# Kernel tuning notes

Hardware: AMD Instinct MI355X
Metric: run time of the kernel (lower is better)

Reference implementation:

```python
import jax, jax.numpy as jnp
import numpy as np

CR = 64                      # cond_repeat
DILS = tuple(2 ** i for _ in range(2) for i in range(10))  # 2 blocks x 10 layers
Q_ZERO = 128


def setup_inputs() -> dict:
    key = jax.random.key(0)
    B, C, TE = 8, 64, 8          # batch, cond channels, encoding timesteps
    R, S, Q = 128, 128, 256      # residual, skip, classes
    L = len(DILS)
    ks = jax.random.split(key, 12)
    sc = 0.1
    return {
        "encodings": jax.random.normal(ks[0], (B, C, TE), jnp.float32),
        "first_w": jax.random.normal(ks[1], (R, 1, 2), jnp.float32) * sc,
        "first_b": jnp.zeros((R,), jnp.float32),
        "causal_w": jax.random.normal(ks[2], (L, 2 * R, R, 2), jnp.float32) * sc,
        "causal_b": jnp.zeros((L, 2 * R), jnp.float32),
        "cond_w": jax.random.normal(ks[3], (L, 2 * R, C), jnp.float32) * sc,
        "cond_b": jnp.zeros((L, 2 * R), jnp.float32),
        "res_w": jax.random.normal(ks[4], (L, R, R), jnp.float32) * sc,
        "res_b": jnp.zeros((L, R), jnp.float32),
        "skip_w": jax.random.normal(ks[5], (L, S, R), jnp.float32) * sc,
        "skip_b": jnp.zeros((L, S), jnp.float32),
        "skipc_w": jax.random.normal(ks[6], (S, R), jnp.float32) * sc,
        "skipc_b": jnp.zeros((S,), jnp.float32),
        "fc_w": jax.random.normal(ks[7], (S, S), jnp.float32) * sc,
        "fc_b": jnp.zeros((S,), jnp.float32),
        "condf_w": jax.random.normal(ks[8], (S, C), jnp.float32) * sc,
        "condf_b": jnp.zeros((S,), jnp.float32),
        "logits_w": jax.random.normal(ks[9], (Q, S), jnp.float32) * sc,
        "logits_b": jnp.zeros((Q,), jnp.float32),
    }


def _generate(encodings, first_w, first_b, causal_w, causal_b, cond_w, cond_b,
              res_w, res_b, skip_w, skip_b, skipc_w, skipc_b, fc_w, fc_b,
              condf_w, condf_b, logits_w, logits_b):
    B = encodings.shape[0]
    R = res_w.shape[1]
    T = encodings.shape[2] * CR

    # ring buffers emulate QueuedConv1d (queue length = dilation, zero-initialized)
    buf_first0 = jnp.zeros((B, 1), jnp.float32)
    bufs0 = tuple(jnp.zeros((B, d, R), jnp.float32) for d in DILS)
    sample0 = jnp.full((B,), Q_ZERO, jnp.int32)

    def step(carry, t):
        sample, buf_first, bufs = carry
        x = sample.astype(jnp.float32) / 255.0 - 0.5                      # [B]
        c = jax.lax.dynamic_index_in_dim(encodings, t // CR, axis=2,
                                         keepdims=False)                  # [B,C]
        # first causal conv (1 -> R, kernel 2): tap0 on delayed sample, tap1 on current
        prev0 = buf_first[:, 0]
        buf_first = buf_first.at[:, 0].set(x)
        res = (prev0[:, None] * first_w[None, :, 0, 0]
               + x[:, None] * first_w[None, :, 0, 1] + first_b)           # [B,R]
        skip = res @ skipc_w.T + skipc_b                                  # [B,S]
        new_bufs = []
        for l, d in enumerate(DILS):
            idx = jnp.mod(t, d)
            prev = jax.lax.dynamic_index_in_dim(bufs[l], idx, axis=1, keepdims=False)
            new_bufs.append(jax.lax.dynamic_update_index_in_dim(bufs[l], res, idx, axis=1))
            z = (prev @ causal_w[l, :, :, 0].T + res @ causal_w[l, :, :, 1].T
                 + causal_b[l] + c @ cond_w[l].T + cond_b[l])             # [B,2R]
            gate, out = jnp.split(z, 2, axis=1)
            h = jax.nn.sigmoid(gate) * jnp.tanh(out)                      # [B,R]
            res = res + h @ res_w[l].T + res_b[l]
            skip = skip + h @ skip_w[l].T + skip_b[l]
        s = jax.nn.relu(skip) @ fc_w.T + fc_b + c @ condf_w.T + condf_b
        logits = jax.nn.relu(s) @ logits_w.T + logits_b                   # [B,Q]
        sample = jnp.argmax(logits, axis=1).astype(jnp.int32)             # 'max' sampling
        return (sample, buf_first, tuple(new_bufs)), (sample, logits)

    _, (samples, logits) = jax.lax.scan(step, (sample0, buf_first0, bufs0),
                                        jnp.arange(T))
    return samples, logits  # [T,B] int32, [T,B,Q] float32


def reference(encodings, first_w, first_b, causal_w, causal_b, cond_w, cond_b,
              res_w, res_b, skip_w, skip_b, skipc_w, skipc_b, fc_w, fc_b,
              condf_w, condf_b, logits_w, logits_b):
    return _generate(encodings, first_w, first_b, causal_w, causal_b, cond_w, cond_b,
                     res_w, res_b, skip_w, skip_b, skipc_w, skipc_b, fc_w, fc_b,
                     condf_w, condf_b, logits_w, logits_b)
```

## Files before the change

### kernel.cpp

```cpp
#include <hip/hip_runtime.h>
#include <math.h>

#define BB 8
#define TT 512
#define LL 20
#define NBLK 64
#define NTHR 256

typedef float f4 __attribute__((ext_vector_type(4)));
typedef unsigned long long ull;

__constant__ int c_dil[LL] = {1,2,4,8,16,32,64,128,256,512,
                              1,2,4,8,16,32,64,128,256,512};
__constant__ int c_roff[LL] = {-1,0,4096,12288,28672,61440,126976,258048,520192,1044480,
                               2093056,2095104,2099200,2107392,2123776,2156544,
                               2222080,2353152,2615296,3139584};

constexpr size_t OFF_RING = 0;
constexpr size_t OFF_X    = 4188160;

#define P_WC     0
#define P_F      20480
#define P_WST    30208
#define P_WSKIPC 30720
#define P_WFC    30976
#define P_WLOG   31232
#define P_WF0    31744
#define P_WF1    31872
#define P_FB     32000
#define P_CONDZ  32128
#define P_SFC    32768
#define P_RESB   32784
#define P_SKIPB  32824
#define P_ZB     32864
#define P_LOGB   32944
#define P_SKIPCB 32948
#define P_XCUR   32950
#define P_XPREV  32958
#define P_XNEW   32966
#define P_SZ     32976
#define P_SL     33008
#define P_SKACC  33040
#define P_R2     33056
#define P_CF     33072
#define P_PREVF  33600
#define P_HF     34656
#define P_RESF   35712
#define P_RES0   36768
#define POOL_FL  38880

__device__ __forceinline__ f4 ldx(const f4* p) {
    f4 r;
    asm volatile("global_load_dwordx4 %0, %1, off sc0 sc1\n\ts_waitcnt vmcnt(0)"
                 : "=v"(r) : "v"(p) : "memory");
    return r;
}
__device__ __forceinline__ void ldx2(const f4* p0, const f4* p1, f4& a, f4& b) {
    asm volatile("global_load_dwordx4 %0, %2, off sc0 sc1\n\t"
                 "global_load_dwordx4 %1, %3, off sc0 sc1\n\t"
                 "s_waitcnt vmcnt(0)"
                 : "=v"(a), "=v"(b) : "v"(p0), "v"(p1) : "memory");
}
__device__ __forceinline__ void stx(f4* p, f4 v) {
    asm volatile("s_waitcnt vmcnt(0)\n\t"
                 "global_store_dwordx4 %0, %1, off sc0 sc1"
                 :: "v"(p), "v"(v) : "memory");
}

__device__ __forceinline__ void publish16(f4* slot, int J, const float* sl, int e) {
    if (threadIdx.x < 6) {
        int q = threadIdx.x;
        f4 v;
        v.x = sl[3*q];
        v.y = (3*q+1 < 16) ? sl[3*q+1] : 0.f;
        v.z = (3*q+2 < 16) ? sl[3*q+2] : 0.f;
        v.w = __int_as_float(e);
        stx(slot + J*6 + q, v);
    }
}
__device__ __forceinline__ void scat16(float* dst, f4 v, int vi, bool dorelu) {
    int j = vi / 6, q = vi - 6*j;
    #pragma unroll
    for (int i = 0; i < 3; ++i) {
        int E = 3*q + i;
        if (E < 16) {
            float x = v[i];
            if (dorelu) x = fmaxf(x, 0.f);
            dst[(E & 7)*132 + 2*j + (E >> 3)] = x;
        }
    }
}
__device__ __forceinline__ void consume16(const f4* slot, int e, float* dst, bool dorelu) {
    int m = threadIdx.x;
    const f4 *p0 = slot + m, *p1 = slot + 256 + m;
    f4 a, b;
    bool two = (m < 128);
    if (two) ldx2(p0, p1, a, b); else a = ldx(p0);
    while (__float_as_int(a.w) != e) { __builtin_amdgcn_s_sleep(1); a = ldx(p0); }
    if (two) { while (__float_as_int(b.w) != e) { __builtin_amdgcn_s_sleep(1); b = ldx(p1); } }
    scat16(dst, a, m, dorelu);
    if (two) scat16(dst, b, m + 256, dorelu);
}
__device__ __forceinline__ void publish32(f4* slot, int J, const float* sl, int e) {
    if (threadIdx.x < 11) {
        int q = threadIdx.x;
        f4 v;
        v.x = sl[3*q];
        v.y = (3*q+1 < 32) ? sl[3*q+1] : 0.f;
        v.z = (3*q+2 < 32) ? sl[3*q+2] : 0.f;
        v.w = __int_as_float(e);
        stx(slot + J*11 + q, v);
    }
}
__device__ __forceinline__ void scat32(float* dst, f4 v, int vi) {
    int j = vi / 11, q = vi - 11*j;
    #pragma unroll
    for (int i = 0; i < 3; ++i) {
        int E = 3*q + i;
        if (E < 32) dst[(E & 7)*260 + 4*j + (E >> 3)] = v[i];
    }
}
__device__ __forceinline__ void consume32(const f4* slot, int e, float* dst) {
    int m = threadIdx.x;
    const f4 *p0 = slot + m, *p1 = slot + 256 + m, *p2 = slot + 512 + m;
    f4 a, b, c;
    ldx2(p0, p1, a, b);
    bool three = (m < 192);
    if (three) c = ldx(p2);
    while (__float_as_int(a.w) != e) { __builtin_amdgcn_s_sleep(1); a = ldx(p0); }
    while (__float_as_int(b.w) != e) { __builtin_amdgcn_s_sleep(1); b = ldx(p1); }
    if (three) { while (__float_as_int(c.w) != e) { __builtin_amdgcn_s_sleep(1); c = ldx(p2); } }
    scat32(dst, a, m);
    scat32(dst, b, m + 256);
    if (three) scat32(dst, c, m + 512);
}

__global__ __launch_bounds__(NTHR, 1) void wn_gen(
    const float* __restrict__ enc,
    const float* __restrict__ first_w,  const float* __restrict__ first_b,
    const float* __restrict__ causal_w, const float* __restrict__ causal_b,
    const float* __restrict__ cond_w,   const float* __restrict__ cond_b,
    const float* __restrict__ res_w,    const float* __restrict__ res_b,
    const float* __restrict__ skip_w,   const float* __restrict__ skip_b,
    const float* __restrict__ skipc_w,  const float* __restrict__ skipc_b,
    const float* __restrict__ fc_w,     const float* __restrict__ fc_b,
    const float* __restrict__ condf_w,  const float* __restrict__ condf_b,
    const float* __restrict__ logits_w, const float* __restrict__ logits_b,
    float* __restrict__ wsf, float* __restrict__ out)
{
    extern __shared__ float pool[];
    const int tid = threadIdx.x;
    const int J = blockIdx.x;
    float* ring = wsf + OFF_RING;
    f4* xb = (f4*)(wsf + OFF_X);

    for (int m = tid; m < 20480; m += NTHR) {
        int l = m >> 10, rem = m & 1023, g = rem >> 8, i = rem & 255;
        int grow = (g < 2) ? (2*J + g) : (128 + 2*J + (g - 2));
        int col = i & 127, k = i >> 7;
        pool[P_WC + m] = causal_w[((size_t)(l*256 + grow)*128 + col)*2 + k];
    }
    if (tid < 256) {
        int r = tid >> 7, i = tid & 127;
        pool[P_WSKIPC + tid] = skipc_w[(size_t)(2*J + r)*128 + i];
        pool[P_WFC + tid]    = fc_w[(size_t)(2*J + r)*128 + i];
    }
    for (int m = tid; m < 512; m += NTHR) {
        int w = m >> 7, i = m & 127;
        pool[P_WLOG + m] = logits_w[(size_t)(4*J + w)*128 + i];
    }
    if (tid < 128) {
        pool[P_WF0 + tid] = first_w[2*tid];
        pool[P_WF1 + tid] = first_w[2*tid + 1];
        pool[P_FB + tid]  = first_b[tid];
    }
    if (tid < 40) {
        int l = tid >> 1, r = tid & 1;
        pool[P_RESB + tid]  = res_b[l*128 + 2*J + r];
        pool[P_SKIPB + tid] = skip_b[l*128 + 2*J + r];
    }
    if (tid < 4) pool[P_LOGB + tid] = logits_b[4*J + tid];
    if (tid < 2) pool[P_SKIPCB + tid] = skipc_b[2*J + tid];
    for (int m = tid; m < 2112; m += NTHR) pool[P_RES0 + m] = 0.f;
    if (tid < 8) { pool[P_XCUR + tid] = 128.f/255.f - 0.5f; pool[P_XPREV + tid] = 0.f; }
    __syncthreads();

    for (int l = 0; l < 19; ++l) {
        for (int m = tid; m < 512; m += NTHR) {
            int g = m >> 7, j = m & 127;
            const float* w1 = pool + P_WC + ((l+1)*4 + g)*256 + 128;
            const float* rw = res_w + (size_t)l*128*128 + j;
            float acc = 0.f;
            #pragma unroll 8
            for (int i = 0; i < 128; ++i) acc += w1[i] * rw[(size_t)i*128];
            pool[P_F + (l*4 + g)*128 + j] = acc;
        }
    }
    if (tid < 80) {
        int l = tid >> 2, g = tid & 3;
        float acc = 0.f;
        if (l >= 1) {
            const float* w1 = pool + P_WC + (l*4 + g)*256 + 128;
            for (int i = 0; i < 128; ++i) acc += w1[i] * res_b[(l-1)*128 + i];
        }
        pool[P_ZB + tid] = acc;
    }
    __syncthreads();

    int e = 0;
    int er_pending = 0;

    for (int t = 0; t < TT; ++t) {
        if ((t & 63) == 0) {
            int te = t >> 6;
            for (int m = tid; m < 512; m += NTHR) {
                int b = m >> 6, j = m & 63;
                pool[P_CF + b*66 + j] = enc[(size_t)b*512 + j*8 + te];
            }
            __syncthreads();
            for (int m = tid; m < 640; m += NTHR) {
                int l = m >> 5, rem = m & 31, g = rem >> 3, b = rem & 7;
                int grow = (g < 2) ? (2*J + g) : (128 + 2*J + (g - 2));
                float acc = causal_b[l*256 + grow] + cond_b[l*256 + grow]
                          + pool[P_ZB + l*4 + g];
                const float* cw = cond_w + (size_t)(l*256 + grow)*64;
                const float* cf = pool + P_CF + b*66;
                for (int j = 0; j < 64; ++j) acc += cw[j]*cf[j];
                pool[P_CONDZ + l*32 + g*8 + b] = acc;
            }
            if (tid < 16) {
                int r = tid >> 3, b = tid & 7, row = 2*J + r;
                float acc = fc_b[row] + condf_b[row];
                const float* cw = condf_w + (size_t)row*64;
                const float* cf = pool + P_CF + b*66;
                for (int j = 0; j < 64; ++j) acc += cw[j]*cf[j];
                pool[P_SFC + r*8 + b] = acc;
            }
            __syncthreads();
        }

        const int cur = t & 1;
        for (int m = tid; m < 1024; m += NTHR) {
            int b = m >> 7, r = m & 127;
            pool[P_RES0 + cur*1056 + b*132 + r] =
                pool[P_XPREV + b]*pool[P_WF0 + r] + pool[P_XCUR + b]*pool[P_WF1 + r] + pool[P_FB + r];
        }
        __syncthreads();
        {
            int w = tid >> 6, lane = tid & 63, b = lane >> 3, k = lane & 7;
            if (w < 2) {
                const float* wr = pool + P_WSKIPC + w*128;
                const float* rs = pool + P_RES0 + cur*1056 + b*132;
                float acc = 0.f;
                #pragma unroll
                for (int i = 0; i < 16; ++i) { int j = k + 8*i; acc += wr[j]*rs[j]; }
                acc += __shfl_xor(acc,1); acc += __shfl_xor(acc,2); acc += __shfl_xor(acc,4);
                if (k == 0) pool[P_SKACC + w*8 + b] = acc + pool[P_SKIPCB + w];
            }
        }
        if (tid < 16) {
            int r = tid >> 3, b = tid & 7;
            pool[P_R2 + r*8 + b] = pool[P_RES0 + cur*1056 + b*132 + 2*J + r];
        }

        for (int l = 0; l < LL; ++l) {
            {
                int g = tid >> 6, lane = tid & 63, b = lane >> 3, k = lane & 7;
                const float* w0 = pool + P_WC + (l*4 + g)*256;
                const float* pv = ((l == 0) ? pool + P_RES0 + (cur^1)*1056 : pool + P_PREVF) + b*132;
                const float* rs = ((l <= 1) ? pool + P_RES0 + cur*1056 : pool + P_RESF) + b*132;
                float acc = 0.f;
                #pragma unroll
                for (int i = 0; i < 16; ++i) {
                    int j = k + 8*i;
                    acc += w0[j]*pv[j] + w0[128 + j]*rs[j];
                }
                if (l >= 1) {
                    const float* fm = pool + P_F + ((l-1)*4 + g)*128;
                    const float* hh = pool + P_HF + b*132;
                    #pragma unroll
                    for (int i = 0; i < 16; ++i) { int j = k + 8*i; acc += fm[j]*hh[j]; }
                }
                acc += __shfl_xor(acc,1); acc += __shfl_xor(acc,2); acc += __shfl_xor(acc,4);
                if (k == 0) pool[P_SZ + g*8 + b] = acc;
            }
            __syncthreads();
            if (tid < 16) {
                int r = tid & 1, b = tid >> 1;
                float g = pool[P_SZ + r*8 + b]     + pool[P_CONDZ + l*32 + r*8 + b];
                float o = pool[P_SZ + (2+r)*8 + b] + pool[P_CONDZ + l*32 + (2+r)*8 + b];
                pool[P_SL + r*8 + b] = (1.f/(1.f + expf(-g))) * tanhf(o);
            }
            __syncthreads();
            ++e; int eh = e;
            publish16(xb + (size_t)(eh & 3)*768, J, pool + P_SL, eh);
            float wv0, wv1;
            {
                int r0 = tid >> 7, i0 = tid & 127;
                wv0 = res_w [(size_t)(l*128 + 2*J + r0)*128 + i0];
                wv1 = skip_w[(size_t)(l*128 + 2*J + r0)*128 + i0];
            }
            ull pfa = 0, pfb = 0;
            if (l <= 18) {
                int d = c_dil[l+1];
                if (t >= d) {
                    int slot = (t - d) & (2*d - 1);
                    const float* rp = ring + c_roff[l+1] + (size_t)slot*1024 + tid*4;
                    pfa = __hip_atomic_load((const ull*)rp,     __ATOMIC_RELAXED, __HIP_MEMORY_SCOPE_AGENT);
                    pfb = __hip_atomic_load((const ull*)(rp+2), __ATOMIC_RELAXED, __HIP_MEMORY_SCOPE_AGENT);
                }
            }
            if (l >= 1 && l <= 18)
                consume16(xb + (size_t)(er_pending & 3)*768, er_pending, pool + P_RESF, false);
            consume16(xb + (size_t)(eh & 3)*768, eh, pool + P_HF, false);
            pool[P_WST + tid] = wv0;
            pool[P_WST + 256 + tid] = wv1;
            __syncthreads();
            {
                int w = tid >> 6, lane = tid & 63, b = lane >> 3, k = lane & 7;
                int r = w & 1, isSkip = w >> 1;
                if (isSkip || l <= 18) {
                    const float* wr = pool + P_WST + (isSkip ? 256 : 0) + r*128;
                    const float* hh = pool + P_HF + b*132;
                    float acc = 0.f;
                    #pragma unroll
                    for (int i = 0; i < 16; ++i) { int j = k + 8*i; acc += wr[j]*hh[j]; }
                    acc += __shfl_xor(acc,1); acc += __shfl_xor(acc,2); acc += __shfl_xor(acc,4);
                    if (k == 0) {
                        if (isSkip) {
                            pool[P_SKACC + r*8 + b] += acc + pool[P_SKIPB + l*2 + r];
                        } else {
                            float v = pool[P_R2 + r*8 + b] + acc + pool[P_RESB + l*2 + r];
                            pool[P_R2 + r*8 + b] = v;
                            pool[P_SL + r*8 + b] = v;
                            int d = c_dil[l+1];
                            int slot = t & (2*d - 1);
                            float* wp = ring + c_roff[l+1] + (size_t)slot*1024 + b*128 + 2*J + r;
                            __hip_atomic_store(wp, v, __ATOMIC_RELAXED, __HIP_MEMORY_SCOPE_AGENT);
                        }
                    }
                }
            }
            __syncthreads();
            if (l <= 17) {
                ++e;
                publish16(xb + (size_t)(e & 3)*768, J, pool + P_SL, e);
                er_pending = e;
            }
            if (l <= 18) {
                int b = tid >> 5, c = (tid & 31)*4;
                union { ull u; float f[2]; } u0, u1;
                u0.u = pfa; u1.u = pfb;
                float* dp = pool + P_PREVF + b*132 + c;
                dp[0] = u0.f[0]; dp[1] = u0.f[1]; dp[2] = u1.f[0]; dp[3] = u1.f[1];
            }
            __syncthreads();
        }

        ++e;
        publish16(xb + (size_t)(e & 3)*768, J, pool + P_SKACC, e);
        consume16(xb + (size_t)(e & 3)*768, e, pool + P_HF, false);
        __syncthreads();
        {
            int w = tid >> 6, lane = tid & 63, b = lane >> 3, k = lane & 7;
            if (w < 2) {
                const float* wr = pool + P_WFC + w*128;
                const float* sk = pool + P_HF + b*132;
                float acc = 0.f;
                #pragma unroll
                for (int i = 0; i < 16; ++i) { int j = k + 8*i; acc += wr[j]*fmaxf(sk[j], 0.f); }
                acc += __shfl_xor(acc,1); acc += __shfl_xor(acc,2); acc += __shfl_xor(acc,4);
                if (k == 0) pool[P_SL + w*8 + b] = acc + pool[P_SFC + w*8 + b];
            }
        }
        __syncthreads();
        ++e;
        publish16(xb + (size_t)(e & 3)*768, J, pool + P_SL, e);
        consume16(xb + (size_t)(e & 3)*768, e, pool + P_RESF, true);
        __syncthreads();
        {
            int g = tid >> 6, lane = tid & 63, b = lane >> 3, k = lane & 7;
            const float* wr = pool + P_WLOG + g*128;
            const float* sv = pool + P_RESF + b*132;
            float acc = 0.f;
            #pragma unroll
            for (int i = 0; i < 16; ++i) { int j = k + 8*i; acc += wr[j]*sv[j]; }
            acc += __shfl_xor(acc,1); acc += __shfl_xor(acc,2); acc += __shfl_xor(acc,4);
            if (k == 0) {
                float v = acc + pool[P_LOGB + g];
                pool[P_SZ + g*8 + b] = v;
                out[4096 + ((size_t)(t*BB + b))*256 + 4*J + g] = v;
            }
        }
        __syncthreads();
        ++e;
        publish32(xb + (size_t)(e & 3)*768, J, pool + P_SZ, e);
        consume32(xb + (size_t)(e & 3)*768, e, pool + P_PREVF);
        __syncthreads();
        {
            int b = tid >> 5, j = tid & 31;
            float best = -3.4e38f; int bi = 0;
            for (int s = 0; s < 8; ++s) {
                int q = s*32 + j;
                float v = pool[P_PREVF + b*260 + q];
                if (v > best) { best = v; bi = q; }
            }
            for (int m = 16; m >= 1; m >>= 1) {
                float ov = __shfl_xor(best, m, 32);
                int   oi = __shfl_xor(bi, m, 32);
                if (ov > best || (ov == best && oi < bi)) { best = ov; bi = oi; }
            }
            if (j == 0) {
                pool[P_XNEW + b] = (float)bi;
                if (J == 0) out[t*BB + b] = (float)bi;
            }
        }
        __syncthreads();
        if (tid < 8) {
            pool[P_XPREV + tid] = pool[P_XCUR + tid];
            pool[P_XCUR + tid]  = pool[P_XNEW + tid]*(1.f/255.f) - 0.5f;
        }
        __syncthreads();
    }
}

extern "C" void kernel_launch(void* const* d_in, const int* in_sizes, int n_in,
                              void* d_out, int out_size, void* d_ws, size_t ws_size,
                              hipStream_t stream) {
    const float* enc      = (const float*)d_in[0];
    const float* first_w  = (const float*)d_in[1];
    const float* first_b  = (const float*)d_in[2];
    const float* causal_w = (const float*)d_in[3];
    const float* causal_b = (const float*)d_in[4];
    const float* cond_w   = (const float*)d_in[5];
    const float* cond_b   = (const float*)d_in[6];
    const float* res_w    = (const float*)d_in[7];
    const float* res_b    = (const float*)d_in[8];
    const float* skip_w   = (const float*)d_in[9];
    const float* skip_b   = (const float*)d_in[10];
    const float* skipc_w  = (const float*)d_in[11];
    const float* skipc_b  = (const float*)d_in[12];
    const float* fc_w     = (const float*)d_in[13];
    const float* fc_b     = (const float*)d_in[14];
    const float* condf_w  = (const float*)d_in[15];
    const float* condf_b  = (const float*)d_in[16];
    const float* logits_w = (const float*)d_in[17];
    const float* logits_b = (const float*)d_in[18];

    float* wsf = (float*)d_ws;
    float* out = (float*)d_out;

    wn_gen<<<NBLK, NTHR, POOL_FL*4, stream>>>(
        enc, first_w, first_b, causal_w, causal_b, cond_w, cond_b,
        res_w, res_b, skip_w, skip_b, skipc_w, skipc_b, fc_w, fc_b,
        condf_w, condf_b, logits_w, logits_b, wsf, out);
}
```

Measured before the change: 37.41 ms.

## Rewrite generator as one block per batch element with no inter-block sync

The old kernel split output channels across 64 blocks and exchanged activations through global-memory flag slots on every layer, spinning until each one arrived. It is replaced by 8 blocks of 1024 threads, one per batch element. Each block computes its whole network step locally, streaming weights from global memory or cache and keeping ring buffers per block in workspace. This removes the cross-block handshakes, but each block now reads all weights on every step rather than holding a weight slice in LDS, and only 8 CUs do the work.

```diff
diff --git a/kernel.cpp b/kernel.cpp
--- a/kernel.cpp
+++ b/kernel.cpp
@@ -1,141 +1,43 @@
 #include <hip/hip_runtime.h>
 #include <math.h>
 
-#define BB 8
+
 #define TT 512
-#define LL 20
-#define NBLK 64
-#define NTHR 256
+#define NBLK 8
+#define NTHR 1024
 
 typedef float f4 __attribute__((ext_vector_type(4)));
-typedef unsigned long long ull;
-
-__constant__ int c_dil[LL] = {1,2,4,8,16,32,64,128,256,512,
-                              1,2,4,8,16,32,64,128,256,512};
-__constant__ int c_roff[LL] = {-1,0,4096,12288,28672,61440,126976,258048,520192,1044480,
-                               2093056,2095104,2099200,2107392,2123776,2156544,
-                               2222080,2353152,2615296,3139584};
-
-constexpr size_t OFF_RING = 0;
-constexpr size_t OFF_X    = 4188160;
-
-#define P_WC     0
-#define P_F      20480
-#define P_WST    30208
-#define P_WSKIPC 30720
-#define P_WFC    30976
-#define P_WLOG   31232
-#define P_WF0    31744
-#define P_WF1    31872
-#define P_FB     32000
-#define P_CONDZ  32128
-#define P_SFC    32768
-#define P_RESB   32784
-#define P_SKIPB  32824
-#define P_ZB     32864
-#define P_LOGB   32944
-#define P_SKIPCB 32948
-#define P_XCUR   32950
-#define P_XPREV  32958
-#define P_XNEW   32966
-#define P_SZ     32976
-#define P_SL     33008
-#define P_SKACC  33040
-#define P_R2     33056
-#define P_CF     33072
-#define P_PREVF  33600
-#define P_HF     34656
-#define P_RESF   35712
-#define P_RES0   36768
-#define POOL_FL  38880
-
-__device__ __forceinline__ f4 ldx(const f4* p) {
-    f4 r;
-    asm volatile("global_load_dwordx4 %0, %1, off sc0 sc1\n\ts_waitcnt vmcnt(0)"
-                 : "=v"(r) : "v"(p) : "memory");
-    return r;
+
+__constant__ int c_dil[20]  = {1,2,4,8,16,32,64,128,256,512,
+                               1,2,4,8,16,32,64,128,256,512};
+__constant__ int c_roff[20] = {0,128,384,896,1920,3968,8064,16256,32640,65408,
+                               130944,131072,131328,131840,132864,134912,
+                               139008,147200,163584,196352};
+
+#define CONDZ  0
+#define RESB   5120
+#define SKIPB  7680
+#define SFC    10240
+#define PREV   10368
+#define RES    10624
+#define HH     10752
+#define SKIP   10880
+#define SV     11008
+#define LOG    11136
+#define CVEC   11392
+#define FW0    11456
+#define FW1    11584
+#define FB     11712
+#define SKIPCB 11840
+#define LOGB   11968
+#define XS     12224
+#define PSZ    12240
+
+__device__ __forceinline__ float dot4(f4 w, f4 x) {
+    return w.x*x.x + w.y*x.y + w.z*x.z + w.w*x.w;
 }
-__device__ __forceinline__ void ldx2(const f4* p0, const f4* p1, f4& a, f4& b) {
-    asm volatile("global_load_dwordx4 %0, %2, off sc0 sc1\n\t"
-                 "global_load_dwordx4 %1, %3, off sc0 sc1\n\t"
-                 "s_waitcnt vmcnt(0)"
-                 : "=v"(a), "=v"(b) : "v"(p0), "v"(p1) : "memory");
-}
-__device__ __forceinline__ void stx(f4* p, f4 v) {
-    asm volatile("s_waitcnt vmcnt(0)\n\t"
-                 "global_store_dwordx4 %0, %1, off sc0 sc1"
-                 :: "v"(p), "v"(v) : "memory");
-}
-
-__device__ __forceinline__ void publish16(f4* slot, int J, const float* sl, int e) {
-    if (threadIdx.x < 6) {
-        int q = threadIdx.x;
-        f4 v;
-        v.x = sl[3*q];
-        v.y = (3*q+1 < 16) ? sl[3*q+1] : 0.f;
-        v.z = (3*q+2 < 16) ? sl[3*q+2] : 0.f;
-        v.w = __int_as_float(e);
-        stx(slot + J*6 + q, v);
-    }
-}
-__device__ __forceinline__ void scat16(float* dst, f4 v, int vi, bool dorelu) {
-    int j = vi / 6, q = vi - 6*j;
-    #pragma unroll
-    for (int i = 0; i < 3; ++i) {
-        int E = 3*q + i;
-        if (E < 16) {
-            float x = v[i];
-            if (dorelu) x = fmaxf(x, 0.f);
-            dst[(E & 7)*132 + 2*j + (E >> 3)] = x;
-        }
-    }
-}
-__device__ __forceinline__ void consume16(const f4* slot, int e, float* dst, bool dorelu) {
-    int m = threadIdx.x;
-    const f4 *p0 = slot + m, *p1 = slot + 256 + m;
-    f4 a, b;
-    bool two = (m < 128);
-    if (two) ldx2(p0, p1, a, b); else a = ldx(p0);
-    while (__float_as_int(a.w) != e) { __builtin_amdgcn_s_sleep(1); a = ldx(p0); }
-    if (two) { while (__float_as_int(b.w) != e) { __builtin_amdgcn_s_sleep(1); b = ldx(p1); } }
-    scat16(dst, a, m, dorelu);
-    if (two) scat16(dst, b, m + 256, dorelu);
-}
-__device__ __forceinline__ void publish32(f4* slot, int J, const float* sl, int e) {
-    if (threadIdx.x < 11) {
-        int q = threadIdx.x;
-        f4 v;
-        v.x = sl[3*q];
-        v.y = (3*q+1 < 32) ? sl[3*q+1] : 0.f;
-        v.z = (3*q+2 < 32) ? sl[3*q+2] : 0.f;
-        v.w = __int_as_float(e);
-        stx(slot + J*11 + q, v);
-    }
-}
-__device__ __forceinline__ void scat32(float* dst, f4 v, int vi) {
-    int j = vi / 11, q = vi - 11*j;
-    #pragma unroll
-    for (int i = 0; i < 3; ++i) {
-        int E = 3*q + i;
-        if (E < 32) dst[(E & 7)*260 + 4*j + (E >> 3)] = v[i];
-    }
-}
-__device__ __forceinline__ void consume32(const f4* slot, int e, float* dst) {
-    int m = threadIdx.x;
-    const f4 *p0 = slot + m, *p1 = slot + 256 + m, *p2 = slot + 512 + m;
-    f4 a, b, c;
-    ldx2(p0, p1, a, b);
-    bool three = (m < 192);
-    if (three) c = ldx(p2);
-    while (__float_as_int(a.w) != e) { __builtin_amdgcn_s_sleep(1); a = ldx(p0); }
-    while (__float_as_int(b.w) != e) { __builtin_amdgcn_s_sleep(1); b = ldx(p1); }
-    if (three) { while (__float_as_int(c.w) != e) { __builtin_amdgcn_s_sleep(1); c = ldx(p2); } }
-    scat32(dst, a, m);
-    scat32(dst, b, m + 256);
-    if (three) scat32(dst, c, m + 512);
-}
-
-__global__ __launch_bounds__(NTHR, 1) void wn_gen(
+
+__global__ __launch_bounds__(NTHR, 4) void wn_gen(
     const float* __restrict__ enc,
     const float* __restrict__ first_w,  const float* __restrict__ first_b,
     const float* __restrict__ causal_w, const float* __restrict__ causal_b,
@@ -148,277 +50,187 @@
     const float* __restrict__ logits_w, const float* __restrict__ logits_b,
     float* __restrict__ wsf, float* __restrict__ out)
 {
-    extern __shared__ float pool[];
+    __shared__ __align__(16) float P[PSZ];
     const int tid = threadIdx.x;
-    const int J = blockIdx.x;
-    float* ring = wsf + OFF_RING;
-    f4* xb = (f4*)(wsf + OFF_X);
-
-    for (int m = tid; m < 20480; m += NTHR) {
-        int l = m >> 10, rem = m & 1023, g = rem >> 8, i = rem & 255;
-        int grow = (g < 2) ? (2*J + g) : (128 + 2*J + (g - 2));
-        int col = i & 127, k = i >> 7;
-        pool[P_WC + m] = causal_w[((size_t)(l*256 + grow)*128 + col)*2 + k];
-    }
-    if (tid < 256) {
-        int r = tid >> 7, i = tid & 127;
-        pool[P_WSKIPC + tid] = skipc_w[(size_t)(2*J + r)*128 + i];
-        pool[P_WFC + tid]    = fc_w[(size_t)(2*J + r)*128 + i];
-    }
-    for (int m = tid; m < 512; m += NTHR) {
-        int w = m >> 7, i = m & 127;
-        pool[P_WLOG + m] = logits_w[(size_t)(4*J + w)*128 + i];
+    const int b = blockIdx.x;
+    float* ringb = wsf + (size_t)b * 262144;
+
+    for (int m = tid; m < 2560; m += NTHR) {
+        P[RESB + m]  = res_b[m];
+        P[SKIPB + m] = skip_b[m];
     }
     if (tid < 128) {
-        pool[P_WF0 + tid] = first_w[2*tid];
-        pool[P_WF1 + tid] = first_w[2*tid + 1];
-        pool[P_FB + tid]  = first_b[tid];
+        P[FW0 + tid]    = first_w[2*tid];
+        P[FW1 + tid]    = first_w[2*tid + 1];
+        P[FB + tid]     = first_b[tid];
+        P[SKIPCB + tid] = skipc_b[tid];
     }
-    if (tid < 40) {
-        int l = tid >> 1, r = tid & 1;
-        pool[P_RESB + tid]  = res_b[l*128 + 2*J + r];
-        pool[P_SKIPB + tid] = skip_b[l*128 + 2*J + r];
-    }
-    if (tid < 4) pool[P_LOGB + tid] = logits_b[4*J + tid];
-    if (tid < 2) pool[P_SKIPCB + tid] = skipc_b[2*J + tid];
-    for (int m = tid; m < 2112; m += NTHR) pool[P_RES0 + m] = 0.f;
-    if (tid < 8) { pool[P_XCUR + tid] = 128.f/255.f - 0.5f; pool[P_XPREV + tid] = 0.f; }
+    if (tid < 256) P[LOGB + tid] = logits_b[tid];
+    if (tid == 0) { P[XS] = 128.f/255.f - 0.5f; P[XS+1] = 0.f; }
     __syncthreads();
-
-    for (int l = 0; l < 19; ++l) {
-        for (int m = tid; m < 512; m += NTHR) {
-            int g = m >> 7, j = m & 127;
-            const float* w1 = pool + P_WC + ((l+1)*4 + g)*256 + 128;
-            const float* rw = res_w + (size_t)l*128*128 + j;
-            float acc = 0.f;
-            #pragma unroll 8
-            for (int i = 0; i < 128; ++i) acc += w1[i] * rw[(size_t)i*128];
-            pool[P_F + (l*4 + g)*128 + j] = acc;
-        }
-    }
-    if (tid < 80) {
-        int l = tid >> 2, g = tid & 3;
-        float acc = 0.f;
-        if (l >= 1) {
-            const float* w1 = pool + P_WC + (l*4 + g)*256 + 128;
-            for (int i = 0; i < 128; ++i) acc += w1[i] * res_b[(l-1)*128 + i];
-        }
-        pool[P_ZB + tid] = acc;
-    }
-    __syncthreads();
-
-    int e = 0;
-    int er_pending = 0;
 
     for (int t = 0; t < TT; ++t) {
         if ((t & 63) == 0) {
-            int te = t >> 6;
-            for (int m = tid; m < 512; m += NTHR) {
-                int b = m >> 6, j = m & 63;
-                pool[P_CF + b*66 + j] = enc[(size_t)b*512 + j*8 + te];
-            }
-            __syncthreads();
-            for (int m = tid; m < 640; m += NTHR) {
-                int l = m >> 5, rem = m & 31, g = rem >> 3, b = rem & 7;
-                int grow = (g < 2) ? (2*J + g) : (128 + 2*J + (g - 2));
-                float acc = causal_b[l*256 + grow] + cond_b[l*256 + grow]
-                          + pool[P_ZB + l*4 + g];
-                const float* cw = cond_w + (size_t)(l*256 + grow)*64;
-                const float* cf = pool + P_CF + b*66;
-                for (int j = 0; j < 64; ++j) acc += cw[j]*cf[j];
-                pool[P_CONDZ + l*32 + g*8 + b] = acc;
-            }
-            if (tid < 16) {
-                int r = tid >> 3, b = tid & 7, row = 2*J + r;
-                float acc = fc_b[row] + condf_b[row];
-                const float* cw = condf_w + (size_t)row*64;
-                const float* cf = pool + P_CF + b*66;
-                for (int j = 0; j < 64; ++j) acc += cw[j]*cf[j];
-                pool[P_SFC + r*8 + b] = acc;
-            }
-            __syncthreads();
-        }
-
-        const int cur = t & 1;
-        for (int m = tid; m < 1024; m += NTHR) {
-            int b = m >> 7, r = m & 127;
-            pool[P_RES0 + cur*1056 + b*132 + r] =
-                pool[P_XPREV + b]*pool[P_WF0 + r] + pool[P_XCUR + b]*pool[P_WF1 + r] + pool[P_FB + r];
-        }
-        __syncthreads();
+            const int te = t >> 6;
+            if (tid < 64) P[CVEC + tid] = enc[(size_t)(b*64 + tid)*8 + te];
+            __syncthreads();
+            {
+                const f4* c4 = (const f4*)&P[CVEC];
+                #pragma unroll
+                for (int ph = 0; ph < 5; ++ph) {
+                    int row = ph*1024 + tid;
+                    const f4* w4 = (const f4*)(cond_w + (size_t)row*64);
+                    float acc = causal_b[row] + cond_b[row];
+                    #pragma unroll 4
+                    for (int k = 0; k < 16; ++k) acc += dot4(w4[k], c4[k]);
+                    P[CONDZ + row] = acc;
+                }
+                if (tid < 128) {
+                    const f4* w4 = (const f4*)(condf_w + (size_t)tid*64);
+                    float acc = fc_b[tid] + condf_b[tid];
+                    #pragma unroll 4
+                    for (int k = 0; k < 16; ++k) acc += dot4(w4[k], c4[k]);
+                    P[SFC + tid] = acc;
+                }
+            }
+            __syncthreads();
+        }
+
+        const int lane6 = tid & 63, wv = tid >> 6;
+
+        if (tid < 128)
+            P[RES + tid] = P[XS+1]*P[FW0+tid] + P[XS]*P[FW1+tid] + P[FB+tid];
+        if (lane6 >= 2 && lane6 < 4) {
+            int k = wv*2 + (lane6 - 2);
+            f4 v = {0.f, 0.f, 0.f, 0.f};
+            if (t >= 1) v = *(const f4*)(ringb + 4*k);
+            *(f4*)&P[PREV + 4*k] = v;
+        }
+        __syncthreads();
+
         {
-            int w = tid >> 6, lane = tid & 63, b = lane >> 3, k = lane & 7;
-            if (w < 2) {
-                const float* wr = pool + P_WSKIPC + w*128;
-                const float* rs = pool + P_RES0 + cur*1056 + b*132;
-                float acc = 0.f;
+            int r = tid >> 3, cc = tid & 7;
+            const f4* w4 = (const f4*)(skipc_w + (size_t)r*128 + cc*16);
+            const f4* x4 = (const f4*)&P[RES + cc*16];
+            float acc = 0.f;
+            #pragma unroll
+            for (int k = 0; k < 4; ++k) acc += dot4(w4[k], x4[k]);
+            acc += __shfl_xor(acc, 1); acc += __shfl_xor(acc, 2); acc += __shfl_xor(acc, 4);
+            if (cc == 0) P[SKIP + r] = acc + P[SKIPCB + r];
+        }
+        __syncthreads();
+
+        for (int l = 0; l < 20; ++l) {
+            const int par = l & 1;
+            {
+                if (lane6 < 2) {
+                    int k = wv*2 + lane6;
+                    int d = c_dil[l], slot = t & (d - 1);
+                    *(f4*)(ringb + c_roff[l] + (size_t)slot*128 + 4*k) =
+                        *(const f4*)&P[RES + 4*k];
+                } else if (lane6 < 4 && l < 19) {
+                    int k = wv*2 + (lane6 - 2);
+                    int d = c_dil[l+1], slot = t & (d - 1);
+                    f4 v = {0.f, 0.f, 0.f, 0.f};
+                    if (t >= d)
+                        v = *(const f4*)(ringb + c_roff[l+1] + (size_t)slot*128 + 4*k);
+                    *(f4*)&P[PREV + (par^1)*128 + 4*k] = v;
+                }
+                int p = tid >> 3, cc = tid & 7;
+                const f4* wg4 = (const f4*)(causal_w + (size_t)(l*256 + p)*256 + cc*32);
+                const f4* wo4 = wg4 + 128*64;
+                const f4* pv4 = (const f4*)&P[PREV + par*128 + cc*16];
+                const f4* rv4 = (const f4*)&P[RES + cc*16];
+                float accg = 0.f, acco = 0.f;
                 #pragma unroll
-                for (int i = 0; i < 16; ++i) { int j = k + 8*i; acc += wr[j]*rs[j]; }
-                acc += __shfl_xor(acc,1); acc += __shfl_xor(acc,2); acc += __shfl_xor(acc,4);
-                if (k == 0) pool[P_SKACC + w*8 + b] = acc + pool[P_SKIPCB + w];
-            }
-        }
-        if (tid < 16) {
-            int r = tid >> 3, b = tid & 7;
-            pool[P_R2 + r*8 + b] = pool[P_RES0 + cur*1056 + b*132 + 2*J + r];
-        }
-
-        for (int l = 0; l < LL; ++l) {
+                for (int k = 0; k < 4; ++k) {
+                    f4 pa = pv4[k], ra = rv4[k];
+                    f4 g0 = wg4[2*k], g1 = wg4[2*k+1];
+                    f4 o0 = wo4[2*k], o1 = wo4[2*k+1];
+                    accg += g0.x*pa.x + g0.y*ra.x + g0.z*pa.y + g0.w*ra.y;
+                    accg += g1.x*pa.z + g1.y*ra.z + g1.z*pa.w + g1.w*ra.w;
+                    acco += o0.x*pa.x + o0.y*ra.x + o0.z*pa.y + o0.w*ra.y;
+                    acco += o1.x*pa.z + o1.y*ra.z + o1.z*pa.w + o1.w*ra.w;
+                }
+                accg += __shfl_xor(accg, 1); accg += __shfl_xor(accg, 2); accg += __shfl_xor(accg, 4);
+                acco += __shfl_xor(acco, 1); acco += __shfl_xor(acco, 2); acco += __shfl_xor(acco, 4);
+                if (cc == 0) {
+                    float g = accg + P[CONDZ + l*256 + p];
+                    float o = acco + P[CONDZ + l*256 + 128 + p];
+                    P[HH + p] = (1.f/(1.f + expf(-g))) * tanhf(o);
+                }
+            }
+            __syncthreads();
             {
-                int g = tid >> 6, lane = tid & 63, b = lane >> 3, k = lane & 7;
-                const float* w0 = pool + P_WC + (l*4 + g)*256;
-                const float* pv = ((l == 0) ? pool + P_RES0 + (cur^1)*1056 : pool + P_PREVF) + b*132;
-                const float* rs = ((l <= 1) ? pool + P_RES0 + cur*1056 : pool + P_RESF) + b*132;
-                float acc = 0.f;
-                #pragma unroll
-                for (int i = 0; i < 16; ++i) {
-                    int j = k + 8*i;
-                    acc += w0[j]*pv[j] + w0[128 + j]*rs[j];
-                }
-                if (l >= 1) {
-                    const float* fm = pool + P_F + ((l-1)*4 + g)*128;
-                    const float* hh = pool + P_HF + b*132;
-                    #pragma unroll
-                    for (int i = 0; i < 16; ++i) { int j = k + 8*i; acc += fm[j]*hh[j]; }
-                }
-                acc += __shfl_xor(acc,1); acc += __shfl_xor(acc,2); acc += __shfl_xor(acc,4);
-                if (k == 0) pool[P_SZ + g*8 + b] = acc;
-            }
-            __syncthreads();
-            if (tid < 16) {
-                int r = tid & 1, b = tid >> 1;
-                float g = pool[P_SZ + r*8 + b]     + pool[P_CONDZ + l*32 + r*8 + b];
-                float o = pool[P_SZ + (2+r)*8 + b] + pool[P_CONDZ + l*32 + (2+r)*8 + b];
-                pool[P_SL + r*8 + b] = (1.f/(1.f + expf(-g))) * tanhf(o);
-            }
-            __syncthreads();
-            ++e; int eh = e;
-            publish16(xb + (size_t)(eh & 3)*768, J, pool + P_SL, eh);
-            float wv0, wv1;
-            {
-                int r0 = tid >> 7, i0 = tid & 127;
-                wv0 = res_w [(size_t)(l*128 + 2*J + r0)*128 + i0];
-                wv1 = skip_w[(size_t)(l*128 + 2*J + r0)*128 + i0];
-            }
-            ull pfa = 0, pfb = 0;
-            if (l <= 18) {
-                int d = c_dil[l+1];
-                if (t >= d) {
-                    int slot = (t - d) & (2*d - 1);
-                    const float* rp = ring + c_roff[l+1] + (size_t)slot*1024 + tid*4;
-                    pfa = __hip_atomic_load((const ull*)rp,     __ATOMIC_RELAXED, __HIP_MEMORY_SCOPE_AGENT);
-                    pfb = __hip_atomic_load((const ull*)(rp+2), __ATOMIC_RELAXED, __HIP_MEMORY_SCOPE_AGENT);
-                }
-            }
-            if (l >= 1 && l <= 18)
-                consume16(xb + (size_t)(er_pending & 3)*768, er_pending, pool + P_RESF, false);
-            consume16(xb + (size_t)(eh & 3)*768, eh, pool + P_HF, false);
-            pool[P_WST + tid] = wv0;
-            pool[P_WST + 256 + tid] = wv1;
-            __syncthreads();
-            {
-                int w = tid >> 6, lane = tid & 63, b = lane >> 3, k = lane & 7;
-                int r = w & 1, isSkip = w >> 1;
-                if (isSkip || l <= 18) {
-                    const float* wr = pool + P_WST + (isSkip ? 256 : 0) + r*128;
-                    const float* hh = pool + P_HF + b*132;
-                    float acc = 0.f;
-                    #pragma unroll
-                    for (int i = 0; i < 16; ++i) { int j = k + 8*i; acc += wr[j]*hh[j]; }
-                    acc += __shfl_xor(acc,1); acc += __shfl_xor(acc,2); acc += __shfl_xor(acc,4);
-                    if (k == 0) {
-                        if (isSkip) {
-                            pool[P_SKACC + r*8 + b] += acc + pool[P_SKIPB + l*2 + r];
-                        } else {
-                            float v = pool[P_R2 + r*8 + b] + acc + pool[P_RESB + l*2 + r];
-                            pool[P_R2 + r*8 + b] = v;
-                            pool[P_SL + r*8 + b] = v;
-                            int d = c_dil[l+1];
-                            int slot = t & (2*d - 1);
-                            float* wp = ring + c_roff[l+1] + (size_t)slot*1024 + b*128 + 2*J + r;
-                            __hip_atomic_store(wp, v, __ATOMIC_RELAXED, __HIP_MEMORY_SCOPE_AGENT);
-                        }
-                    }
-                }
-            }
-            __syncthreads();
-            if (l <= 17) {
-                ++e;
-                publish16(xb + (size_t)(e & 3)*768, J, pool + P_SL, e);
-                er_pending = e;
-            }
-            if (l <= 18) {
-                int b = tid >> 5, c = (tid & 31)*4;
-                union { ull u; float f[2]; } u0, u1;
-                u0.u = pfa; u1.u = pfb;
-                float* dp = pool + P_PREVF + b*132 + c;
-                dp[0] = u0.f[0]; dp[1] = u0.f[1]; dp[2] = u1.f[0]; dp[3] = u1.f[1];
-            }
-            __syncthreads();
-        }
-
-        ++e;
-        publish16(xb + (size_t)(e & 3)*768, J, pool + P_SKACC, e);
-        consume16(xb + (size_t)(e & 3)*768, e, pool + P_HF, false);
-        __syncthreads();
+                int r = tid >> 3, cc = tid & 7;
+                const f4* h4 = (const f4*)&P[HH + cc*16];
+                f4 h0 = h4[0], h1 = h4[1], h2 = h4[2], h3 = h4[3];
+                const f4* sw4 = (const f4*)(skip_w + ((size_t)l*128 + r)*128 + cc*16);
+                float acs = dot4(sw4[0], h0) + dot4(sw4[1], h1)
+                          + dot4(sw4[2], h2) + dot4(sw4[3], h3);
+                acs += __shfl_xor(acs, 1); acs += __shfl_xor(acs, 2); acs += __shfl_xor(acs, 4);
+                if (l < 19) {
+                    const f4* rw4 = (const f4*)(res_w + ((size_t)l*128 + r)*128 + cc*16);
+                    float acr = dot4(rw4[0], h0) + dot4(rw4[1], h1)
+                              + dot4(rw4[2], h2) + dot4(rw4[3], h3);
+                    acr += __shfl_xor(acr, 1); acr += __shfl_xor(acr, 2); acr += __shfl_xor(acr, 4);
+                    if (cc == 0) P[RES + r] += acr + P[RESB + l*128 + r];
+                }
+                if (cc == 0) P[SKIP + r] += acs + P[SKIPB + l*128 + r];
+            }
+            __syncthreads();
+        }
+
         {
-            int w = tid >> 6, lane = tid & 63, b = lane >> 3, k = lane & 7;
-            if (w < 2) {
-                const float* wr = pool + P_WFC + w*128;
-                const float* sk = pool + P_HF + b*132;
-                float acc = 0.f;
-                #pragma unroll
-                for (int i = 0; i < 16; ++i) { int j = k + 8*i; acc += wr[j]*fmaxf(sk[j], 0.f); }
-                acc += __shfl_xor(acc,1); acc += __shfl_xor(acc,2); acc += __shfl_xor(acc,4);
-                if (k == 0) pool[P_SL + w*8 + b] = acc + pool[P_SFC + w*8 + b];
-            }
-        }
-        __syncthreads();
-        ++e;
-        publish16(xb + (size_t)(e & 3)*768, J, pool + P_SL, e);
-        consume16(xb + (size_t)(e & 3)*768, e, pool + P_RESF, true);
+            int r = tid >> 3, cc = tid & 7;
+            const f4* w4 = (const f4*)(fc_w + (size_t)r*128 + cc*16);
+            const f4* k4 = (const f4*)&P[SKIP + cc*16];
+            float acc = 0.f;
+            #pragma unroll
+            for (int k = 0; k < 4; ++k) {
+                f4 w = w4[k], x = k4[k];
+                acc += w.x*fmaxf(x.x, 0.f) + w.y*fmaxf(x.y, 0.f)
+                     + w.z*fmaxf(x.z, 0.f) + w.w*fmaxf(x.w, 0.f);
+            }
+            acc += __shfl_xor(acc, 1); acc += __shfl_xor(acc, 2); acc += __shfl_xor(acc, 4);
+            if (cc == 0) P[SV + r] = fmaxf(acc + P[SFC + r], 0.f);
+        }
         __syncthreads();
         {
-            int g = tid >> 6, lane = tid & 63, b = lane >> 3, k = lane & 7;
-            const float* wr = pool + P_WLOG + g*128;
-            const float* sv = pool + P_RESF + b*132;
+            int q = tid >> 2, c2 = tid & 3;
+            const f4* w4 = (const f4*)(logits_w + (size_t)q*128 + c2*32);
+            const f4* s4 = (const f4*)&P[SV + c2*32];
             float acc = 0.f;
             #pragma unroll
-            for (int i = 0; i < 16; ++i) { int j = k + 8*i; acc += wr[j]*sv[j]; }
-            acc += __shfl_xor(acc,1); acc += __shfl_xor(acc,2); acc += __shfl_xor(acc,4);
-            if (k == 0) {
-                float v = acc + pool[P_LOGB + g];
-                pool[P_SZ + g*8 + b] = v;
-                out[4096 + ((size_t)(t*BB + b))*256 + 4*J + g] = v;
-            }
-        }
-        __syncthreads();
-        ++e;
-        publish32(xb + (size_t)(e & 3)*768, J, pool + P_SZ, e);
-        consume32(xb + (size_t)(e & 3)*768, e, pool + P_PREVF);
-        __syncthreads();
-        {
-            int b = tid >> 5, j = tid & 31;
+            for (int k = 0; k < 8; ++k) acc += dot4(w4[k], s4[k]);
+            acc += __shfl_xor(acc, 1); acc += __shfl_xor(acc, 2);
+            if (c2 == 0) P[LOG + q] = acc + P[LOGB + q];
+        }
+        __syncthreads();
+        if (tid < 64) {
             float best = -3.4e38f; int bi = 0;
-            for (int s = 0; s < 8; ++s) {
-                int q = s*32 + j;
-                float v = pool[P_PREVF + b*260 + q];
+            #pragma unroll
+            for (int s0 = 0; s0 < 4; ++s0) {
+                int q = s0*64 + tid;
+                float v = P[LOG + q];
                 if (v > best) { best = v; bi = q; }
             }
-            for (int m = 16; m >= 1; m >>= 1) {
-                float ov = __shfl_xor(best, m, 32);
-                int   oi = __shfl_xor(bi, m, 32);
+            #pragma unroll
+            for (int m = 32; m >= 1; m >>= 1) {
+                float ov = __shfl_xor(best, m);
+                int   oi = __shfl_xor(bi, m);
                 if (ov > best || (ov == best && oi < bi)) { best = ov; bi = oi; }
             }
-            if (j == 0) {
-                pool[P_XNEW + b] = (float)bi;
-                if (J == 0) out[t*BB + b] = (float)bi;
-            }
-        }
-        __syncthreads();
-        if (tid < 8) {
-            pool[P_XPREV + tid] = pool[P_XCUR + tid];
-            pool[P_XCUR + tid]  = pool[P_XNEW + tid]*(1.f/255.f) - 0.5f;
+            if (tid == 0) {
+                float nb = (float)bi;
+                out[t*8 + b] = nb;
+                P[XS+1] = P[XS];
+                P[XS]   = nb*(1.f/255.f) - 0.5f;
+            }
+        } else if (tid < 128) {
+            int k = tid - 64;
+            *(f4*)(out + 4096 + ((size_t)(t*8 + b))*256 + 4*k) =
+                *(const f4*)&P[LOG + 4*k];
         }
         __syncthreads();
     }
@@ -450,7 +262,7 @@
     float* wsf = (float*)d_ws;
     float* out = (float*)d_out;
 
-    wn_gen<<<NBLK, NTHR, POOL_FL*4, stream>>>(
+    wn_gen<<<NBLK, NTHR, 0, stream>>>(
         enc, first_w, first_b, causal_w, causal_b, cond_w, cond_b,
         res_w, res_b, skip_w, skip_b, skipc_w, skipc_b, fc_w, fc_b,
         condf_w, condf_b, logits_w, logits_b, wsf, out);
```

Result: slower. 127.1 ms (+239.8%).
